# Kernel tuning notes

Hardware: AMD Instinct MI355X
Metric: run time of the kernel (lower is better)

The kernel has to match this reference:

```python
import jax, jax.numpy as jnp
import numpy as np

N = 10000          # num nodes
E = 160000         # num edges (before self-loops)
F_IN = 50          # PPI num_features
N_CLS = 121        # PPI num_classes
HID = 128          # hidden_channels
NEG_SLOPE = 0.2    # PyG GATConv leaky_relu slope


def gat_conv(x, src, dst, W, a_src, a_dst, b, heads, out_ch, concat):
    # x: [N, F_in]; src/dst: [E'] (self-loops already appended)
    h = (x @ W).reshape(N, heads, out_ch)                  # [N,H,C]
    s_src = jnp.sum(h * a_src, axis=-1)                    # [N,H]
    s_dst = jnp.sum(h * a_dst, axis=-1)                    # [N,H]
    alpha = jax.nn.leaky_relu(s_src[src] + s_dst[dst], NEG_SLOPE)  # [E',H]
    # segment softmax over incoming edges of each dst node
    m = jax.ops.segment_max(alpha, dst, num_segments=N)    # [N,H]
    e = jnp.exp(alpha - m[dst])
    denom = jax.ops.segment_sum(e, dst, num_segments=N)    # [N,H]
    coef = e / denom[dst]                                  # [E',H]
    msg = h[src] * coef[:, :, None]                        # [E',H,C]
    out = jax.ops.segment_sum(msg, dst, num_segments=N)    # [N,H,C]
    out = out.reshape(N, heads * out_ch) if concat else out.mean(axis=1)
    return out + b


def setup_inputs() -> dict:
    key = jax.random.key(0)
    ks = jax.random.split(key, 16)
    D = HID * 8  # 1024
    glorot = lambda k, shape: (jax.random.normal(k, shape, jnp.float32)
                               * jnp.sqrt(2.0 / (shape[0] + shape[-1])))
    return {
        "x": jax.random.normal(ks[0], (N, F_IN), jnp.float32),
        "edge_index": jax.random.randint(ks[1], (2, E), 0, N, jnp.int32),
        # layer 1: 50 -> 128, heads=8, concat
        "W1": glorot(ks[2], (F_IN, 8 * HID)),
        "a_src1": glorot(ks[3], (8, HID)),
        "a_dst1": glorot(ks[4], (8, HID)),
        "b1": jnp.zeros((D,), jnp.float32),
        # layer 2: 1024 -> 1024, heads=1, concat
        "W2": glorot(ks[5], (D, D)),
        "a_src2": glorot(ks[6], (1, D)),
        "a_dst2": glorot(ks[7], (1, D)),
        "b2": jnp.zeros((D,), jnp.float32),
        # layer 3: 1024 -> 121, heads=1, concat=False (mean)
        "W3": glorot(ks[8], (D, N_CLS)),
        "a_src3": glorot(ks[9], (1, N_CLS)),
        "a_dst3": glorot(ks[10], (1, N_CLS)),
        "b3": jnp.zeros((N_CLS,), jnp.float32),
    }


def reference(x, edge_index, W1, a_src1, a_dst1, b1, W2, a_src2, a_dst2, b2,
              W3, a_src3, a_dst3, b3):
    # GATConv adds self-loops by default
    loops = jnp.arange(N, dtype=edge_index.dtype)
    src = jnp.concatenate([edge_index[0], loops])
    dst = jnp.concatenate([edge_index[1], loops])

    x1 = gat_conv(x, src, dst, W1, a_src1, a_dst1, b1, 8, HID, True)
    h = jax.nn.elu(x1)  # dropout is identity in eval mode
    x1 = gat_conv(h, src, dst, W2, a_src2, a_dst2, b2, 1, HID * 8, True)
    h = jax.nn.elu(x1)
    x1 = gat_conv(h, src, dst, W3, a_src3, a_dst3, b3, 1, N_CLS, False)
    return x1  # module returns pre-ELU output of last conv
```

## Files before the change

kernel.cpp:

```cpp
#include <hip/hip_runtime.h>
#include <hip/hip_bf16.h>

#define NNODES 10000
#define NEDGES 160000
#define F_IN   50
#define HIDDEN 128
#define NCLS   121
#define DBIG   1024
#define MPAD   10112

typedef __attribute__((ext_vector_type(8))) short short8v;
typedef __attribute__((ext_vector_type(4))) float f32x4;
typedef __attribute__((ext_vector_type(4))) unsigned short u16x4;

#define GLD16(gsrc, ldst) \
  __builtin_amdgcn_global_load_lds((__attribute__((address_space(1))) const void*)(const void*)(gsrc), \
                                   (__attribute__((address_space(3))) void*)(void*)(ldst), 16, 0, 0)

__global__ void hist_kernel(const int* __restrict__ ei, int* __restrict__ cnt,
                            int E_, int N_) {
    int e = blockIdx.x * blockDim.x + threadIdx.x;
    if (e >= E_ + N_) return;
    int dst = (e < E_) ? ei[E_ + e] : (e - E_);
    atomicAdd(&cnt[dst], 1);
}

__global__ void scan_kernel(const int* __restrict__ cnt, int* __restrict__ row_ptr,
                            int n) {
    __shared__ int sums[16];
    __shared__ int stot;
    int tid = threadIdx.x, lane = tid & 63, wid = tid >> 6;
    int running = 0;
    for (int base = 0; base < n; base += 1024) {
        int i = base + tid;
        int v = (i < n) ? cnt[i] : 0;
        int x = v;
        #pragma unroll
        for (int o = 1; o < 64; o <<= 1) {
            int t = __shfl_up(x, o);
            if (lane >= o) x += t;
        }
        if (lane == 63) sums[wid] = x;
        __syncthreads();
        if (tid == 0) {
            int acc = 0;
            #pragma unroll
            for (int k = 0; k < 16; ++k) { int t = sums[k]; sums[k] = acc; acc += t; }
            stot = acc;
        }
        __syncthreads();
        if (i < n) row_ptr[i] = running + sums[wid] + x - v;
        running += stot;
        __syncthreads();
    }
    if (threadIdx.x == 0) row_ptr[n] = running;
}

__global__ void scatter_kernel(const int* __restrict__ ei,
                               const int* __restrict__ row_ptr,
                               int* __restrict__ cursor, int* __restrict__ esrc,
                               int E_, int N_) {
    int e = blockIdx.x * blockDim.x + threadIdx.x;
    if (e >= E_ + N_) return;
    int s, d;
    if (e < E_) { s = ei[e]; d = ei[E_ + e]; } else { s = d = e - E_; }
    int pos = row_ptr[d] + atomicAdd(&cursor[d], 1);
    esrc[pos] = s;
}

__global__ void fold_kernel(const float* __restrict__ W1,
                            const float* __restrict__ a_src,
                            const float* __restrict__ a_dst,
                            float* __restrict__ wfold) {
    int b = blockIdx.x;
    int h = b & 7, which = b >> 3;
    int k = threadIdx.x;
    const float* a = which ? a_dst : a_src;
    float dot = 0.f;
    if (k < F_IN) {
        for (int c = 0; c < HIDDEN; ++c)
            dot += W1[(size_t)k * DBIG + h * HIDDEN + c] * a[h * HIDDEN + c];
    }
    wfold[(which * 8 + h) * 64 + k] = dot;
}

__global__ void sdot1x_kernel(const float* __restrict__ x,
                              const float* __restrict__ wfold,
                              float* __restrict__ ssrc, float* __restrict__ sdst) {
    __shared__ float sh_x[16][52];
    __shared__ float sh_w[16][64];
    int tid = threadIdx.x;
    int n0 = blockIdx.x * 16;
    for (int i = tid; i < 16 * 64; i += 256) sh_w[i >> 6][i & 63] = wfold[i];
    for (int i = tid; i < 16 * F_IN; i += 256) {
        int nl = i / F_IN, k = i % F_IN;
        int n = n0 + nl;
        sh_x[nl][k] = (n < NNODES) ? x[(size_t)n * F_IN + k] : 0.f;
    }
    __syncthreads();
    int nl = tid >> 4, o = tid & 15;
    int n = n0 + nl;
    if (n >= NNODES) return;
    float s = 0.f;
    #pragma unroll
    for (int k = 0; k < F_IN; ++k) s += sh_x[nl][k] * sh_w[o][k];
    if (o < 8) ssrc[n * 8 + o] = s;
    else       sdst[n * 8 + (o - 8)] = s;
}

__global__ void agg1_kernel(const float* __restrict__ x,
                            const float* __restrict__ ssrc,
                            const float* __restrict__ sdst,
                            const int* __restrict__ row_ptr,
                            const int* __restrict__ esrc,
                            __hip_bfloat16* __restrict__ YH,
                            __hip_bfloat16* __restrict__ YL) {
    int n = blockIdx.x;
    int tid = threadIdx.x;
    if (n >= NNODES) {
        #pragma unroll
        for (int h = 0; h < 8; ++h) {
            size_t o = ((size_t)h * MPAD + n) * 64 + tid;
            YH[o] = __float2bfloat16(0.f);
            YL[o] = __float2bfloat16(0.f);
        }
        return;
    }
    __shared__ float m_s[8], inv_s[8], sd_s[8];
    __shared__ int sidx[64];
    __shared__ float coef[64][9];
    int row = row_ptr[n], end = row_ptr[n + 1];
    {
        int el = tid >> 3, hh = tid & 7;
        float sd = sdst[n * 8 + hh];
        float mymax = -1e30f;
        for (int e = row + el; e < end; e += 8) {
            float a = ssrc[esrc[e] * 8 + hh] + sd;
            a = (a >= 0.f) ? a : 0.2f * a;
            mymax = fmaxf(mymax, a);
        }
        #pragma unroll
        for (int o = 8; o < 64; o <<= 1) mymax = fmaxf(mymax, __shfl_xor(mymax, o));
        float mysum = 0.f;
        for (int e = row + el; e < end; e += 8) {
            float a = ssrc[esrc[e] * 8 + hh] + sd;
            a = (a >= 0.f) ? a : 0.2f * a;
            mysum += __expf(a - mymax);
        }
        #pragma unroll
        for (int o = 8; o < 64; o <<= 1) mysum += __shfl_xor(mysum, o);
        if (el == 0) { m_s[hh] = mymax; inv_s[hh] = 1.f / mysum; sd_s[hh] = sd; }
    }
    __syncthreads();
    float acc[8] = {};
    for (int cs = row; cs < end; cs += 64) {
        int nE = min(64, end - cs);
        if (tid < nE) {
            int s = esrc[cs + tid];
            sidx[tid] = s;
            #pragma unroll
            for (int h = 0; h < 8; ++h) {
                float a = ssrc[s * 8 + h] + sd_s[h];
                a = (a >= 0.f) ? a : 0.2f * a;
                coef[tid][h] = __expf(a - m_s[h]) * inv_s[h];
            }
        }
        __syncthreads();
        if (tid < F_IN) {
            for (int i = 0; i < nE; ++i) {
                float xv = x[(size_t)sidx[i] * F_IN + tid];
                #pragma unroll
                for (int h = 0; h < 8; ++h) acc[h] += coef[i][h] * xv;
            }
        }
        __syncthreads();
    }
    #pragma unroll
    for (int h = 0; h < 8; ++h) {
        float v = acc[h];
        __hip_bfloat16 hb = __float2bfloat16(v);
        size_t o = ((size_t)h * MPAD + n) * 64 + tid;
        YH[o] = hb;
        YL[o] = __float2bfloat16(v - __bfloat162float(hb));
    }
}

__global__ void tsplit_kernel(const float* __restrict__ W, int K, int Nn, int Kpad,
                              __hip_bfloat16* __restrict__ bh,
                              __hip_bfloat16* __restrict__ bl) {
    __shared__ float sh[64][65];
    int k0 = blockIdx.x * 64, n0 = blockIdx.y * 64;
    int tid = threadIdx.x;
    int cc = tid & 63, rr = tid >> 6;
    #pragma unroll
    for (int i = 0; i < 16; ++i) {
        int r = rr + i * 4;
        int k = k0 + r, n = n0 + cc;
        sh[r][cc] = (k < K && n < Nn) ? W[(size_t)k * Nn + n] : 0.f;
    }
    __syncthreads();
    #pragma unroll
    for (int i = 0; i < 16; ++i) {
        int r = rr + i * 4;
        float v = sh[cc][r];
        __hip_bfloat16 h = __float2bfloat16(v);
        size_t o = (size_t)(n0 + r) * Kpad + k0 + cc;
        bh[o] = h;
        bl[o] = __float2bfloat16(v - __bfloat162float(h));
    }
}

template <int BM, int BN, int WM, int WN, bool EPI, bool MASKC, bool SDOT>
__global__ __launch_bounds__(256, 4)
void gemm_mfma(const __hip_bfloat16* __restrict__ Ah,
               const __hip_bfloat16* __restrict__ Al, int ldA, long sAz,
               const __hip_bfloat16* __restrict__ Bh,
               const __hip_bfloat16* __restrict__ Bl, int ldB, long sBz,
               float* __restrict__ C, int ldC, int M, int Nn, int K, int colPerZ,
               const float* __restrict__ bias,
               __hip_bfloat16* __restrict__ OH, __hip_bfloat16* __restrict__ OL,
               int swzNB,
               const float* __restrict__ adot_s, const float* __restrict__ adot_d,
               float* __restrict__ sdot_s, float* __restrict__ sdot_d,
               float* __restrict__ zeroPtr, int zeroCnt) {
    constexpr int MF = BM / (WM * 16);
    constexpr int NF = BN / (WN * 16);
    constexpr int TAB = BM * 64;
    constexpr int TBB = BN * 64;
    __shared__ char lds[2 * TAB + 2 * TBB];
    char* sAh = lds;
    char* sAl = lds + TAB;
    char* sBh = lds + 2 * TAB;
    char* sBl = lds + 2 * TAB + TBB;

    const int tid = threadIdx.x;
    if (zeroPtr) {
        int lb = ((blockIdx.z * gridDim.y + blockIdx.y) * gridDim.x + blockIdx.x)
                     * (int)blockDim.x + tid;
        if (lb < zeroCnt) zeroPtr[lb] = 0.f;
    }

    const int z = blockIdx.z;
    Ah += (size_t)z * sAz; Al += (size_t)z * sAz;
    Bh += (size_t)z * sBz; Bl += (size_t)z * sBz;

    int bx = blockIdx.x, by = blockIdx.y;
    if (swzNB) {
        int gx = gridDim.x;
        int lin = by * gx + bx;
        int c = lin & 7, i = lin >> 3;
        int nl = c * (swzNB >> 3) + i;
        bx = nl % gx;
        by = nl / gx;
    }

    const int lane = tid & 63;
    const int w = tid >> 6;
    const int wm = w / WN, wn = w % WN;
    const int row0 = by * BM;
    const int col0 = bx * BN;

    constexpr int nchA = BM / 16, nchB = BN / 16;
    constexpr int NCH = 2 * nchA + 2 * nchB;
    constexpr int NIT = NCH / 4;

    const int Rl = lane >> 3;
    const int sl = lane & 7;
    const int rl = 2 * Rl + (sl >> 2);

    const __hip_bfloat16* gsrc[NIT];
    char* ldsp[NIT];
    #pragma unroll
    for (int it = 0; it < NIT; ++it) {
        int lc = w + it * 4;
        const __hip_bfloat16* g; char* base; int ld; int r0;
        if (lc < nchA)              { g = Ah; base = sAh; ld = ldA; r0 = row0; }
        else if ((lc -= nchA) < nchA){ g = Al; base = sAl; ld = ldA; r0 = row0; }
        else if ((lc -= nchA) < nchB){ g = Bh; base = sBh; ld = ldB; r0 = col0; }
        else { lc -= nchB;            g = Bl; base = sBl; ld = ldB; r0 = col0; }
        int R = lc * 8 + Rl;
        int rowt = lc * 16 + rl;
        int psrc = (sl & 3) ^ (R & 3);
        gsrc[it] = g + (size_t)(r0 + rowt) * ld + psrc * 8;
        ldsp[it] = base + lc * 1024;
    }

    f32x4 acc[MF][NF];
    #pragma unroll
    for (int i = 0; i < MF; ++i)
        #pragma unroll
        for (int j = 0; j < NF; ++j) acc[i][j] = (f32x4){0.f, 0.f, 0.f, 0.f};

    for (int k0 = 0; k0 < K; k0 += 32) {
        __syncthreads();
        #pragma unroll
        for (int it = 0; it < NIT; ++it) {
            GLD16(gsrc[it], ldsp[it]);
            gsrc[it] += 32;
        }
        __syncthreads();
        short8v ah[MF], al[MF];
        #pragma unroll
        for (int mf = 0; mf < MF; ++mf) {
            int r = wm * (BM / WM) + mf * 16 + (lane & 15);
            int p = lane >> 4;
            int off = (r >> 1) * 128 + (r & 1) * 64 + ((p ^ ((r >> 1) & 3)) << 4);
            ah[mf] = *(const short8v*)(sAh + off);
            al[mf] = *(const short8v*)(sAl + off);
        }
        #pragma unroll
        for (int nf = 0; nf < NF; ++nf) {
            int r = wn * (BN / WN) + nf * 16 + (lane & 15);
            int p = lane >> 4;
            int off = (r >> 1) * 128 + (r & 1) * 64 + ((p ^ ((r >> 1) & 3)) << 4);
            short8v bh = *(const short8v*)(sBh + off);
            short8v bl = *(const short8v*)(sBl + off);
            #pragma unroll
            for (int mf = 0; mf < MF; ++mf) {
                acc[mf][nf] = __builtin_amdgcn_mfma_f32_16x16x32_bf16(ah[mf], bh, acc[mf][nf], 0, 0, 0);
                acc[mf][nf] = __builtin_amdgcn_mfma_f32_16x16x32_bf16(ah[mf], bl, acc[mf][nf], 0, 0, 0);
                acc[mf][nf] = __builtin_amdgcn_mfma_f32_16x16x32_bf16(al[mf], bh, acc[mf][nf], 0, 0, 0);
            }
        }
    }

    float ps[MF][4], pd[MF][4];
    if (SDOT) {
        #pragma unroll
        for (int mf = 0; mf < MF; ++mf)
            #pragma unroll
            for (int r2 = 0; r2 < 4; ++r2) { ps[mf][r2] = 0.f; pd[mf][r2] = 0.f; }
    }

    #pragma unroll
    for (int mf = 0; mf < MF; ++mf) {
        int m = row0 + wm * (BM / WM) + mf * 16 + ((lane >> 4) << 2);
        #pragma unroll
        for (int nf = 0; nf < NF; ++nf) {
            int ln = col0 + wn * (BN / WN) + nf * 16 + (lane & 15);
            if (MASKC && ln >= Nn) continue;
            int gcol = z * colPerZ + ln;
            f32x4 v = acc[mf][nf];
            if (SDOT) {
                float as = adot_s[gcol], ad = adot_d[gcol];
                #pragma unroll
                for (int r2 = 0; r2 < 4; ++r2) {
                    ps[mf][r2] += v[r2] * as;
                    pd[mf][r2] += v[r2] * ad;
                }
            }
            if (EPI) {
                float bv = bias[gcol];
                #pragma unroll
                for (int r2 = 0; r2 < 4; ++r2) {
                    if (MASKC && m + r2 >= M) continue;
                    float o = v[r2] + bv;
                    o = (o > 0.f) ? o : __expf(o) - 1.f;
                    __hip_bfloat16 hb = __float2bfloat16(o);
                    size_t idx = (size_t)(m + r2) * ldC + gcol;
                    OH[idx] = hb;
                    OL[idx] = __float2bfloat16(o - __bfloat162float(hb));
                }
            } else {
                #pragma unroll
                for (int r2 = 0; r2 < 4; ++r2) {
                    if (MASKC && m + r2 >= M) continue;
                    C[(size_t)(m + r2) * ldC + gcol] = v[r2];
                }
            }
        }
    }

    if (SDOT) {
        #pragma unroll
        for (int mf = 0; mf < MF; ++mf) {
            #pragma unroll
            for (int r2 = 0; r2 < 4; ++r2) {
                float vs = ps[mf][r2], vd = pd[mf][r2];
                #pragma unroll
                for (int o = 1; o < 16; o <<= 1) {
                    vs += __shfl_xor(vs, o);
                    vd += __shfl_xor(vd, o);
                }
                if ((lane & 15) == 0) {
                    int m = row0 + wm * (BM / WM) + mf * 16 + ((lane >> 4) << 2) + r2;
                    atomicAdd(&sdot_s[m], vs);
                    atomicAdd(&sdot_d[m], vd);
                }
            }
        }
    }
}

template <int C>
__global__ void sdot_kernel(const float* __restrict__ h, int ld,
                            const float* __restrict__ a_src,
                            const float* __restrict__ a_dst,
                            float* __restrict__ ssrc, float* __restrict__ sdst) {
    int n = blockIdx.x;
    int lane = threadIdx.x;
    const float* hp = h + (size_t)n * ld;
    float p1 = 0.f, p2 = 0.f;
    for (int c = lane; c < C; c += 64) {
        float v = hp[c];
        p1 += v * a_src[c];
        p2 += v * a_dst[c];
    }
    #pragma unroll
    for (int off = 32; off; off >>= 1) {
        p1 += __shfl_down(p1, off);
        p2 += __shfl_down(p2, off);
    }
    if (lane == 0) { ssrc[n] = p1; sdst[n] = p2; }
}

__global__ void coef_kernel(const float* __restrict__ ssrc,
                            const float* __restrict__ sdst,
                            const int* __restrict__ row_ptr,
                            const int* __restrict__ esrc,
                            float* __restrict__ coef) {
    int n = blockIdx.x, lane = threadIdx.x;
    int row = row_ptr[n], end = row_ptr[n + 1];
    float sd = sdst[n];
    float mymax = -1e30f;
    for (int e = row + lane; e < end; e += 64) {
        float a = ssrc[esrc[e]] + sd;
        a = (a >= 0.f) ? a : 0.2f * a;
        coef[e] = a;
        mymax = fmaxf(mymax, a);
    }
    #pragma unroll
    for (int o = 32; o; o >>= 1) mymax = fmaxf(mymax, __shfl_xor(mymax, o));
    float mysum = 0.f;
    for (int e = row + lane; e < end; e += 64) {
        float ex = __expf(coef[e] - mymax);
        coef[e] = ex;
        mysum += ex;
    }
    #pragma unroll
    for (int o = 32; o; o >>= 1) mysum += __shfl_xor(mysum, o);
    float inv = 1.f / mysum;
    for (int e = row + lane; e < end; e += 64) coef[e] *= inv;
}

__global__ void sliceagg2_kernel(const float* __restrict__ h,
                                 const float* __restrict__ coef,
                                 const int* __restrict__ row_ptr,
                                 const int* __restrict__ esrc,
                                 const float* __restrict__ bias,
                                 __hip_bfloat16* __restrict__ oh,
                                 __hip_bfloat16* __restrict__ ol,
                                 int ch0) {
    int bx = blockIdx.x;
    int slice = bx & 7, nb = bx >> 3;
    int tid = threadIdx.x;
    int n = nb * 16 + (tid >> 4);
    int j = tid & 15;
    int col = ch0 + slice * 64 + j * 4;
    int row = row_ptr[n], end = row_ptr[n + 1];
    float4 acc = {0.f, 0.f, 0.f, 0.f};
    int e = row;
    for (; e + 4 <= end; e += 4) {
        int s0 = esrc[e], s1 = esrc[e + 1], s2 = esrc[e + 2], s3 = esrc[e + 3];
        float c0 = coef[e], c1 = coef[e + 1], c2 = coef[e + 2], c3 = coef[e + 3];
        const float4 v0 = *reinterpret_cast<const float4*>(h + (size_t)s0 * DBIG + col);
        const float4 v1 = *reinterpret_cast<const float4*>(h + (size_t)s1 * DBIG + col);
        const float4 v2 = *reinterpret_cast<const float4*>(h + (size_t)s2 * DBIG + col);
        const float4 v3 = *reinterpret_cast<const float4*>(h + (size_t)s3 * DBIG + col);
        acc.x += c0 * v0.x + c1 * v1.x + c2 * v2.x + c3 * v3.x;
        acc.y += c0 * v0.y + c1 * v1.y + c2 * v2.y + c3 * v3.y;
        acc.z += c0 * v0.z + c1 * v1.z + c2 * v2.z + c3 * v3.z;
        acc.w += c0 * v0.w + c1 * v1.w + c2 * v2.w + c3 * v3.w;
    }
    for (; e < end; ++e) {
        int s0 = esrc[e];
        float c0 = coef[e];
        const float4 v0 = *reinterpret_cast<const float4*>(h + (size_t)s0 * DBIG + col);
        acc.x += c0 * v0.x; acc.y += c0 * v0.y;
        acc.z += c0 * v0.z; acc.w += c0 * v0.w;
    }
    const float4 bv = *reinterpret_cast<const float4*>(bias + col);
    float vals[4] = {acc.x + bv.x, acc.y + bv.y, acc.z + bv.z, acc.w + bv.w};
    unsigned short hs[4], ls[4];
    #pragma unroll
    for (int r = 0; r < 4; ++r) {
        float o = (vals[r] > 0.f) ? vals[r] : __expf(vals[r]) - 1.f;
        __hip_bfloat16 hb = __float2bfloat16(o);
        hs[r] = __bfloat16_as_ushort(hb);
        ls[r] = __bfloat16_as_ushort(__float2bfloat16(o - __bfloat162float(hb)));
    }
    *(u16x4*)(oh + (size_t)n * DBIG + col) = (u16x4){hs[0], hs[1], hs[2], hs[3]};
    *(u16x4*)(ol + (size_t)n * DBIG + col) = (u16x4){ls[0], ls[1], ls[2], ls[3]};
}

__global__ void sliceagg3_kernel(const float* __restrict__ h,
                                 const float* __restrict__ coef,
                                 const int* __restrict__ row_ptr,
                                 const int* __restrict__ esrc,
                                 const float* __restrict__ bias,
                                 float* __restrict__ out) {
    int bx = blockIdx.x;
    int slice = bx & 1, nb = bx >> 1;
    int tid = threadIdx.x;
    int n = nb * 16 + (tid >> 4);
    int j = tid & 15;
    int col = slice * 64 + j * 4;
    int row = row_ptr[n], end = row_ptr[n + 1];
    float4 acc = {0.f, 0.f, 0.f, 0.f};
    int e = row;
    for (; e + 4 <= end; e += 4) {
        int s0 = esrc[e], s1 = esrc[e + 1], s2 = esrc[e + 2], s3 = esrc[e + 3];
        float c0 = coef[e], c1 = coef[e + 1], c2 = coef[e + 2], c3 = coef[e + 3];
        const float4 v0 = *reinterpret_cast<const float4*>(h + (size_t)s0 * 128 + col);
        const float4 v1 = *reinterpret_cast<const float4*>(h + (size_t)s1 * 128 + col);
        const float4 v2 = *reinterpret_cast<const float4*>(h + (size_t)s2 * 128 + col);
        const float4 v3 = *reinterpret_cast<const float4*>(h + (size_t)s3 * 128 + col);
        acc.x += c0 * v0.x + c1 * v1.x + c2 * v2.x + c3 * v3.x;
        acc.y += c0 * v0.y + c1 * v1.y + c2 * v2.y + c3 * v3.y;
        acc.z += c0 * v0.z + c1 * v1.z + c2 * v2.z + c3 * v3.z;
        acc.w += c0 * v0.w + c1 * v1.w + c2 * v2.w + c3 * v3.w;
    }
    for (; e < end; ++e) {
        int s0 = esrc[e];
        float c0 = coef[e];
        const float4 v0 = *reinterpret_cast<const float4*>(h + (size_t)s0 * 128 + col);
        acc.x += c0 * v0.x; acc.y += c0 * v0.y;
        acc.z += c0 * v0.z; acc.w += c0 * v0.w;
    }
    float vals[4] = {acc.x, acc.y, acc.z, acc.w};
    #pragma unroll
    for (int r = 0; r < 4; ++r) {
        int c = col + r;
        if (c < NCLS) out[(size_t)n * NCLS + c] = vals[r] + bias[c];
    }
}

extern "C" void kernel_launch(void* const* d_in, const int* in_sizes, int n_in,
                              void* d_out, int out_size, void* d_ws, size_t ws_size,
                              hipStream_t stream) {
    const float* x      = (const float*)d_in[0];
    const int*   ei     = (const int*)d_in[1];
    const float* W1     = (const float*)d_in[2];
    const float* a_src1 = (const float*)d_in[3];
    const float* a_dst1 = (const float*)d_in[4];
    const float* b1     = (const float*)d_in[5];
    const float* W2     = (const float*)d_in[6];
    const float* a_src2 = (const float*)d_in[7];
    const float* a_dst2 = (const float*)d_in[8];
    const float* b2     = (const float*)d_in[9];
    const float* W3     = (const float*)d_in[10];
    const float* a_src3 = (const float*)d_in[11];
    const float* a_dst3 = (const float*)d_in[12];
    const float* b3     = (const float*)d_in[13];
    float* out = (float*)d_out;

    const int N = NNODES, E = NEDGES, Etot = NEDGES + NNODES;

    char* p = (char*)d_ws;
    float* H_buf = (float*)p;                 p += (size_t)N * DBIG * 4;
    __hip_bfloat16* AH = (__hip_bfloat16*)p;  p += (size_t)MPAD * DBIG * 2;
    __hip_bfloat16* AL = (__hip_bfloat16*)p;  p += (size_t)MPAD * DBIG * 2;
    __hip_bfloat16* BTH = (__hip_bfloat16*)p; p += (size_t)1024 * 1024 * 2;
    __hip_bfloat16* BTL = (__hip_bfloat16*)p; p += (size_t)1024 * 1024 * 2;
    float* ssrc = (float*)p;                  p += (size_t)N * 8 * 4;
    float* sdst = (float*)p;                  p += (size_t)N * 8 * 4;
    float* wfold = (float*)p;                 p += 16 * 64 * 4;
    int* row_ptr = (int*)p;                   p += 40064;
    int* cursor = (int*)p;                    p += 2 * N * 4;
    int* cursor2 = cursor + N;
    int* esrc = (int*)p;                      p += (size_t)Etot * 4;
    float* coef = (float*)p;                  p += (size_t)Etot * 4;
    __hip_bfloat16* YH = (__hip_bfloat16*)H_buf;
    __hip_bfloat16* YL = YH + (size_t)8 * MPAD * 64;
    float* H3 = (float*)H_buf;

    hipMemsetAsync(cursor, 0, 2 * N * sizeof(int), stream);
    hist_kernel<<<(Etot + 255) / 256, 256, 0, stream>>>(ei, cursor, E, N);
    scan_kernel<<<1, 1024, 0, stream>>>(cursor, row_ptr, N);
    scatter_kernel<<<(Etot + 255) / 256, 256, 0, stream>>>(ei, row_ptr, cursor2, esrc, E, N);

    fold_kernel<<<16, 64, 0, stream>>>(W1, a_src1, a_dst1, wfold);
    sdot1x_kernel<<<(N + 15) / 16, 256, 0, stream>>>(x, wfold, ssrc, sdst);
    agg1_kernel<<<MPAD, 64, 0, stream>>>(x, ssrc, sdst, row_ptr, esrc, YH, YL);
    {
        dim3 tg(1, 16);
        tsplit_kernel<<<tg, 256, 0, stream>>>(W1, F_IN, DBIG, 64, BTH, BTL);
        dim3 grid(1, MPAD / 128, 8);
        gemm_mfma<128, 128, 2, 2, true, true, false><<<grid, 256, 0, stream>>>(
            YH, YL, 64, (long)MPAD * 64, BTH, BTL, 64, (long)HIDDEN * 64,
            nullptr, DBIG, MPAD, HIDDEN, 64, HIDDEN, b1, AH, AL, 0,
            nullptr, nullptr, nullptr, nullptr, ssrc, 2 * N * 8);
    }
    {
        dim3 tg(16, 16);
        tsplit_kernel<<<tg, 256, 0, stream>>>(W2, DBIG, DBIG, DBIG, BTH, BTL);
        dim3 grid(DBIG / 128, MPAD / 128, 1);
        gemm_mfma<128, 128, 2, 2, false, true, true><<<grid, 256, 0, stream>>>(
            AH, AL, DBIG, 0, BTH, BTL, DBIG, 0,
            H_buf, DBIG, N, DBIG, DBIG, 0, nullptr, nullptr, nullptr, 632,
            a_src2, a_dst2, ssrc, sdst, nullptr, 0);
        coef_kernel<<<N, 64, 0, stream>>>(ssrc, sdst, row_ptr, esrc, coef);
        sliceagg2_kernel<<<8 * (N / 16), 256, 0, stream>>>(
            H_buf, coef, row_ptr, esrc, b2, AH, AL, 0);
        sliceagg2_kernel<<<8 * (N / 16), 256, 0, stream>>>(
            H_buf, coef, row_ptr, esrc, b2, AH, AL, 512);
    }
    {
        dim3 tg(16, 2);
        tsplit_kernel<<<tg, 256, 0, stream>>>(W3, DBIG, NCLS, DBIG, BTH, BTL);
        dim3 grid(4, MPAD / 64, 1);
        gemm_mfma<64, 32, 2, 2, false, false, false><<<grid, 256, 0, stream>>>(
            AH, AL, DBIG, 0, BTH, BTL, DBIG, 0,
            H3, 128, MPAD, 128, DBIG, 0, nullptr, nullptr, nullptr, 632,
            nullptr, nullptr, nullptr, nullptr, nullptr, 0);
        sdot_kernel<NCLS><<<N, 64, 0, stream>>>(H3, 128, a_src3, a_dst3, ssrc, sdst);
        coef_kernel<<<N, 64, 0, stream>>>(ssrc, sdst, row_ptr, esrc, coef);
        sliceagg3_kernel<<<2 * (N / 16), 256, 0, stream>>>(
            H3, coef, row_ptr, esrc, b3, out);
    }
}
```

Baseline: 288.7 us.

## Add specialized 2-wave layer-2 GEMM and pack edge source with coefficient

```diff
diff --git a/kernel.cpp b/kernel.cpp
--- a/kernel.cpp
+++ b/kernel.cpp
@@ -392,6 +392,138 @@
     }
 }
 
+__global__ __launch_bounds__(128, 2)
+void gemm2_mfma(const __hip_bfloat16* __restrict__ Ah,
+                const __hip_bfloat16* __restrict__ Al,
+                const __hip_bfloat16* __restrict__ Bh,
+                const __hip_bfloat16* __restrict__ Bl,
+                float* __restrict__ C, int M,
+                const float* __restrict__ adot_s, const float* __restrict__ adot_d,
+                float* __restrict__ sdot_s, float* __restrict__ sdot_d,
+                int swzNB) {
+    constexpr int TAB = 128 * 64;
+    __shared__ char lds[4 * TAB];
+    char* sAh = lds;
+    char* sAl = lds + TAB;
+    char* sBh = lds + 2 * TAB;
+    char* sBl = lds + 3 * TAB;
+
+    const int tid = threadIdx.x;
+    const int lane = tid & 63;
+    const int w = tid >> 6;
+
+    int bx = blockIdx.x, by = blockIdx.y;
+    {
+        int gx = gridDim.x;
+        int lin = by * gx + bx;
+        int c = lin & 7, i = lin >> 3;
+        int nl = c * (swzNB >> 3) + i;
+        bx = nl % gx;
+        by = nl / gx;
+    }
+    const int row0 = by * 128;
+    const int col0 = bx * 128;
+
+    const int Rl = lane >> 3;
+    const int sl = lane & 7;
+    const int rl = 2 * Rl + (sl >> 2);
+    const int psrc = (sl & 3) ^ (Rl & 3);
+
+    const __hip_bfloat16* pT0 = Ah + (size_t)(row0 + w * 16 + rl) * 1024 + psrc * 8;
+    const __hip_bfloat16* pT1 = Al + (size_t)(row0 + w * 16 + rl) * 1024 + psrc * 8;
+    const __hip_bfloat16* pT2 = Bh + (size_t)(col0 + w * 16 + rl) * 1024 + psrc * 8;
+    const __hip_bfloat16* pT3 = Bl + (size_t)(col0 + w * 16 + rl) * 1024 + psrc * 8;
+    char* l0 = sAh + w * 1024;
+    char* l1 = sAl + w * 1024;
+    char* l2 = sBh + w * 1024;
+    char* l3 = sBl + w * 1024;
+
+    f32x4 acc[4][8];
+    #pragma unroll
+    for (int i = 0; i < 4; ++i)
+        #pragma unroll
+        for (int j = 0; j < 8; ++j) acc[i][j] = (f32x4){0.f, 0.f, 0.f, 0.f};
+
+    for (int k0 = 0; k0 < 1024; k0 += 32) {
+        __syncthreads();
+        #pragma unroll
+        for (int j = 0; j < 4; ++j) {
+            GLD16(pT0 + (size_t)j * 32768, l0 + j * 2048);
+            GLD16(pT1 + (size_t)j * 32768, l1 + j * 2048);
+            GLD16(pT2 + (size_t)j * 32768, l2 + j * 2048);
+            GLD16(pT3 + (size_t)j * 32768, l3 + j * 2048);
+        }
+        pT0 += 32; pT1 += 32; pT2 += 32; pT3 += 32;
+        __syncthreads();
+        short8v ah[4], al[4];
+        #pragma unroll
+        for (int mf = 0; mf < 4; ++mf) {
+            int r = w * 64 + mf * 16 + (lane & 15);
+            int p = lane >> 4;
+            int off = (r >> 1) * 128 + (r & 1) * 64 + ((p ^ ((r >> 1) & 3)) << 4);
+            ah[mf] = *(const short8v*)(sAh + off);
+            al[mf] = *(const short8v*)(sAl + off);
+        }
+        #pragma unroll
+        for (int nf = 0; nf < 8; ++nf) {
+            int r = nf * 16 + (lane & 15);
+            int p = lane >> 4;
+            int off = (r >> 1) * 128 + (r & 1) * 64 + ((p ^ ((r >> 1) & 3)) << 4);
+            short8v bh = *(const short8v*)(sBh + off);
+            short8v bl = *(const short8v*)(sBl + off);
+            #pragma unroll
+            for (int mf = 0; mf < 4; ++mf) {
+                acc[mf][nf] = __builtin_amdgcn_mfma_f32_16x16x32_bf16(ah[mf], bh, acc[mf][nf], 0, 0, 0);
+                acc[mf][nf] = __builtin_amdgcn_mfma_f32_16x16x32_bf16(ah[mf], bl, acc[mf][nf], 0, 0, 0);
+                acc[mf][nf] = __builtin_amdgcn_mfma_f32_16x16x32_bf16(al[mf], bh, acc[mf][nf], 0, 0, 0);
+            }
+        }
+    }
+
+    float ps[4][4], pd[4][4];
+    #pragma unroll
+    for (int mf = 0; mf < 4; ++mf)
+        #pragma unroll
+        for (int r2 = 0; r2 < 4; ++r2) { ps[mf][r2] = 0.f; pd[mf][r2] = 0.f; }
+
+    #pragma unroll
+    for (int mf = 0; mf < 4; ++mf) {
+        int m = row0 + w * 64 + mf * 16 + ((lane >> 4) << 2);
+        #pragma unroll
+        for (int nf = 0; nf < 8; ++nf) {
+            int gcol = col0 + nf * 16 + (lane & 15);
+            f32x4 v = acc[mf][nf];
+            float as = adot_s[gcol], ad = adot_d[gcol];
+            #pragma unroll
+            for (int r2 = 0; r2 < 4; ++r2) {
+                ps[mf][r2] += v[r2] * as;
+                pd[mf][r2] += v[r2] * ad;
+            }
+            #pragma unroll
+            for (int r2 = 0; r2 < 4; ++r2) {
+                if (m + r2 < M) C[(size_t)(m + r2) * 1024 + gcol] = v[r2];
+            }
+        }
+    }
+    #pragma unroll
+    for (int mf = 0; mf < 4; ++mf) {
+        #pragma unroll
+        for (int r2 = 0; r2 < 4; ++r2) {
+            float vs = ps[mf][r2], vd = pd[mf][r2];
+            #pragma unroll
+            for (int o = 1; o < 16; o <<= 1) {
+                vs += __shfl_xor(vs, o);
+                vd += __shfl_xor(vd, o);
+            }
+            if ((lane & 15) == 0) {
+                int m = row0 + w * 64 + mf * 16 + ((lane >> 4) << 2) + r2;
+                atomicAdd(&sdot_s[m], vs);
+                atomicAdd(&sdot_d[m], vd);
+            }
+        }
+    }
+}
+
 template <int C>
 __global__ void sdot_kernel(const float* __restrict__ h, int ld,
                             const float* __restrict__ a_src,
@@ -418,35 +550,37 @@
                             const float* __restrict__ sdst,
                             const int* __restrict__ row_ptr,
                             const int* __restrict__ esrc,
-                            float* __restrict__ coef) {
+                            int2* __restrict__ ecp) {
     int n = blockIdx.x, lane = threadIdx.x;
     int row = row_ptr[n], end = row_ptr[n + 1];
     float sd = sdst[n];
     float mymax = -1e30f;
     for (int e = row + lane; e < end; e += 64) {
-        float a = ssrc[esrc[e]] + sd;
+        int s = esrc[e];
+        float a = ssrc[s] + sd;
         a = (a >= 0.f) ? a : 0.2f * a;
-        coef[e] = a;
+        ecp[e].x = s;
+        ecp[e].y = __float_as_int(a);
         mymax = fmaxf(mymax, a);
     }
     #pragma unroll
     for (int o = 32; o; o >>= 1) mymax = fmaxf(mymax, __shfl_xor(mymax, o));
     float mysum = 0.f;
     for (int e = row + lane; e < end; e += 64) {
-        float ex = __expf(coef[e] - mymax);
-        coef[e] = ex;
+        float ex = __expf(__int_as_float(ecp[e].y) - mymax);
+        ecp[e].y = __float_as_int(ex);
         mysum += ex;
     }
     #pragma unroll
     for (int o = 32; o; o >>= 1) mysum += __shfl_xor(mysum, o);
     float inv = 1.f / mysum;
-    for (int e = row + lane; e < end; e += 64) coef[e] *= inv;
+    for (int e = row + lane; e < end; e += 64)
+        ecp[e].y = __float_as_int(__int_as_float(ecp[e].y) * inv);
 }
 
 __global__ void sliceagg2_kernel(const float* __restrict__ h,
-                                 const float* __restrict__ coef,
+                                 const int2* __restrict__ ecp,
                                  const int* __restrict__ row_ptr,
-                                 const int* __restrict__ esrc,
                                  const float* __restrict__ bias,
                                  __hip_bfloat16* __restrict__ oh,
                                  __hip_bfloat16* __restrict__ ol,
@@ -461,21 +595,22 @@
     float4 acc = {0.f, 0.f, 0.f, 0.f};
     int e = row;
     for (; e + 4 <= end; e += 4) {
-        int s0 = esrc[e], s1 = esrc[e + 1], s2 = esrc[e + 2], s3 = esrc[e + 3];
-        float c0 = coef[e], c1 = coef[e + 1], c2 = coef[e + 2], c3 = coef[e + 3];
-        const float4 v0 = *reinterpret_cast<const float4*>(h + (size_t)s0 * DBIG + col);
-        const float4 v1 = *reinterpret_cast<const float4*>(h + (size_t)s1 * DBIG + col);
-        const float4 v2 = *reinterpret_cast<const float4*>(h + (size_t)s2 * DBIG + col);
-        const float4 v3 = *reinterpret_cast<const float4*>(h + (size_t)s3 * DBIG + col);
+        int2 p0 = ecp[e], p1 = ecp[e + 1], p2 = ecp[e + 2], p3 = ecp[e + 3];
+        float c0 = __int_as_float(p0.y), c1 = __int_as_float(p1.y);
+        float c2 = __int_as_float(p2.y), c3 = __int_as_float(p3.y);
+        const float4 v0 = *reinterpret_cast<const float4*>(h + (size_t)p0.x * DBIG + col);
+        const float4 v1 = *reinterpret_cast<const float4*>(h + (size_t)p1.x * DBIG + col);
+        const float4 v2 = *reinterpret_cast<const float4*>(h + (size_t)p2.x * DBIG + col);
+        const float4 v3 = *reinterpret_cast<const float4*>(h + (size_t)p3.x * DBIG + col);
         acc.x += c0 * v0.x + c1 * v1.x + c2 * v2.x + c3 * v3.x;
         acc.y += c0 * v0.y + c1 * v1.y + c2 * v2.y + c3 * v3.y;
         acc.z += c0 * v0.z + c1 * v1.z + c2 * v2.z + c3 * v3.z;
         acc.w += c0 * v0.w + c1 * v1.w + c2 * v2.w + c3 * v3.w;
     }
     for (; e < end; ++e) {
-        int s0 = esrc[e];
-        float c0 = coef[e];
-        const float4 v0 = *reinterpret_cast<const float4*>(h + (size_t)s0 * DBIG + col);
+        int2 p0 = ecp[e];
+        float c0 = __int_as_float(p0.y);
+        const float4 v0 = *reinterpret_cast<const float4*>(h + (size_t)p0.x * DBIG + col);
         acc.x += c0 * v0.x; acc.y += c0 * v0.y;
         acc.z += c0 * v0.z; acc.w += c0 * v0.w;
     }
@@ -494,9 +629,8 @@
 }
 
 __global__ void sliceagg3_kernel(const float* __restrict__ h,
-                                 const float* __restrict__ coef,
+                                 const int2* __restrict__ ecp,
                                  const int* __restrict__ row_ptr,
-                                 const int* __restrict__ esrc,
                                  const float* __restrict__ bias,
                                  float* __restrict__ out) {
     int bx = blockIdx.x;
@@ -509,21 +643,22 @@
     float4 acc = {0.f, 0.f, 0.f, 0.f};
     int e = row;
     for (; e + 4 <= end; e += 4) {
-        int s0 = esrc[e], s1 = esrc[e + 1], s2 = esrc[e + 2], s3 = esrc[e + 3];
-        float c0 = coef[e], c1 = coef[e + 1], c2 = coef[e + 2], c3 = coef[e + 3];
-        const float4 v0 = *reinterpret_cast<const float4*>(h + (size_t)s0 * 128 + col);
-        const float4 v1 = *reinterpret_cast<const float4*>(h + (size_t)s1 * 128 + col);
-        const float4 v2 = *reinterpret_cast<const float4*>(h + (size_t)s2 * 128 + col);
-        const float4 v3 = *reinterpret_cast<const float4*>(h + (size_t)s3 * 128 + col);
+        int2 p0 = ecp[e], p1 = ecp[e + 1], p2 = ecp[e + 2], p3 = ecp[e + 3];
+        float c0 = __int_as_float(p0.y), c1 = __int_as_float(p1.y);
+        float c2 = __int_as_float(p2.y), c3 = __int_as_float(p3.y);
+        const float4 v0 = *reinterpret_cast<const float4*>(h + (size_t)p0.x * 128 + col);
+        const float4 v1 = *reinterpret_cast<const float4*>(h + (size_t)p1.x * 128 + col);
+        const float4 v2 = *reinterpret_cast<const float4*>(h + (size_t)p2.x * 128 + col);
+        const float4 v3 = *reinterpret_cast<const float4*>(h + (size_t)p3.x * 128 + col);
         acc.x += c0 * v0.x + c1 * v1.x + c2 * v2.x + c3 * v3.x;
         acc.y += c0 * v0.y + c1 * v1.y + c2 * v2.y + c3 * v3.y;
         acc.z += c0 * v0.z + c1 * v1.z + c2 * v2.z + c3 * v3.z;
         acc.w += c0 * v0.w + c1 * v1.w + c2 * v2.w + c3 * v3.w;
     }
     for (; e < end; ++e) {
-        int s0 = esrc[e];
-        float c0 = coef[e];
-        const float4 v0 = *reinterpret_cast<const float4*>(h + (size_t)s0 * 128 + col);
+        int2 p0 = ecp[e];
+        float c0 = __int_as_float(p0.y);
+        const float4 v0 = *reinterpret_cast<const float4*>(h + (size_t)p0.x * 128 + col);
         acc.x += c0 * v0.x; acc.y += c0 * v0.y;
         acc.z += c0 * v0.z; acc.w += c0 * v0.w;
     }
@@ -569,7 +704,7 @@
     int* cursor = (int*)p;                    p += 2 * N * 4;
     int* cursor2 = cursor + N;
     int* esrc = (int*)p;                      p += (size_t)Etot * 4;
-    float* coef = (float*)p;                  p += (size_t)Etot * 4;
+    int2* ecp = (int2*)p;                     p += (size_t)Etot * 8;
     __hip_bfloat16* YH = (__hip_bfloat16*)H_buf;
     __hip_bfloat16* YL = YH + (size_t)8 * MPAD * 64;
     float* H3 = (float*)H_buf;
@@ -594,16 +729,14 @@
     {
         dim3 tg(16, 16);
         tsplit_kernel<<<tg, 256, 0, stream>>>(W2, DBIG, DBIG, DBIG, BTH, BTL);
-        dim3 grid(DBIG / 128, MPAD / 128, 1);
-        gemm_mfma<128, 128, 2, 2, false, true, true><<<grid, 256, 0, stream>>>(
-            AH, AL, DBIG, 0, BTH, BTL, DBIG, 0,
-            H_buf, DBIG, N, DBIG, DBIG, 0, nullptr, nullptr, nullptr, 632,
-            a_src2, a_dst2, ssrc, sdst, nullptr, 0);
-        coef_kernel<<<N, 64, 0, stream>>>(ssrc, sdst, row_ptr, esrc, coef);
+        dim3 grid(DBIG / 128, MPAD / 128);
+        gemm2_mfma<<<grid, 128, 0, stream>>>(
+            AH, AL, BTH, BTL, H_buf, N, a_src2, a_dst2, ssrc, sdst, 632);
+        coef_kernel<<<N, 64, 0, stream>>>(ssrc, sdst, row_ptr, esrc, ecp);
         sliceagg2_kernel<<<8 * (N / 16), 256, 0, stream>>>(
-            H_buf, coef, row_ptr, esrc, b2, AH, AL, 0);
+            H_buf, ecp, row_ptr, b2, AH, AL, 0);
         sliceagg2_kernel<<<8 * (N / 16), 256, 0, stream>>>(
-            H_buf, coef, row_ptr, esrc, b2, AH, AL, 512);
+            H_buf, ecp, row_ptr, b2, AH, AL, 512);
     }
     {
         dim3 tg(16, 2);
@@ -614,8 +747,8 @@
             H3, 128, MPAD, 128, DBIG, 0, nullptr, nullptr, nullptr, 632,
             nullptr, nullptr, nullptr, nullptr, nullptr, 0);
         sdot_kernel<NCLS><<<N, 64, 0, stream>>>(H3, 128, a_src3, a_dst3, ssrc, sdst);
-        coef_kernel<<<N, 64, 0, stream>>>(ssrc, sdst, row_ptr, esrc, coef);
+        coef_kernel<<<N, 64, 0, stream>>>(ssrc, sdst, row_ptr, esrc, ecp);
         sliceagg3_kernel<<<2 * (N / 16), 256, 0, stream>>>(
-            H3, coef, row_ptr, esrc, b3, out);
-    }
-}
+            H3, ecp, row_ptr, b3, out);
+    }
+}
```

Measured after the change: 296.9 us. 2.8% more time.
